# Kernel optimization log

Hardware: AMD Instinct MI355X
Metric: run time of the kernel (lower is better)

## Reference

```python
import jax, jax.numpy as jnp
import numpy as np

B, IN, H = 4096, 1024, 1024

def setup_inputs() -> dict:
    key = jax.random.key(0)
    ks = jax.random.split(key, 7)
    s_in = 1.0 / np.sqrt(IN)
    s_h = 1.0 / np.sqrt(H)
    return {
        "x": jax.random.normal(ks[0], (B, IN), dtype=jnp.float32),
        "h": jax.random.normal(ks[1], (B, H), dtype=jnp.float32),
        "W_ih": jax.random.uniform(ks[2], (3 * H, IN), jnp.float32, -s_in, s_in),
        "b_ih": jax.random.uniform(ks[3], (3 * H,), jnp.float32, -s_in, s_in),
        "W_rzh": jax.random.uniform(ks[4], (2 * H, H), jnp.float32, -s_h, s_h),
        "W_nh": jax.random.uniform(ks[5], (H, H), jnp.float32, -s_h, s_h),
        "b_nh": jax.random.uniform(ks[6], (H,), jnp.float32, -s_h, s_h),
    }


def reference(x, h, W_ih, b_ih, W_rzh, W_nh, b_nh):
    # Input projection: one fused matmul producing (B, 3H)
    x_proj = x @ W_ih.T + b_ih
    r_x, z_x, n_x = jnp.split(x_proj, 3, axis=-1)
    # Fused r/z hidden projection (B, 2H)
    rz_h = h @ W_rzh.T
    r_h, z_h = jnp.split(rz_h, 2, axis=-1)
    r = jax.nn.sigmoid(r_x + r_h)
    z = jax.nn.sigmoid(z_x + z_h)
    n = jnp.tanh(n_x + r * (h @ W_nh.T + b_nh))
    return (1.0 - z) * n + z * h
```

## Files before the change

### kernel.cpp

```cpp
#include <hip/hip_runtime.h>
#include <hip/hip_bf16.h>
#include <stdint.h>


typedef __attribute__((ext_vector_type(4))) int i32x4;
typedef __attribute__((ext_vector_type(16))) int i32x16;

#define SX (127.0f / 5.5f)
#define SW 4064.0f
#define INVS (1.0f / (SX * SW))

__device__ __forceinline__ unsigned pack4(const float4 f, float s) {
  int a = __float2int_rn(fminf(fmaxf(f.x * s, -127.f), 127.f));
  int b = __float2int_rn(fminf(fmaxf(f.y * s, -127.f), 127.f));
  int c = __float2int_rn(fminf(fmaxf(f.z * s, -127.f), 127.f));
  int d = __float2int_rn(fminf(fmaxf(f.w * s, -127.f), 127.f));
  return (unsigned)(a & 255) | ((unsigned)(b & 255) << 8) |
         ((unsigned)(c & 255) << 16) | ((unsigned)(d & 255) << 24);
}

__device__ __forceinline__ void cvt16(const float* __restrict__ src, float s,
                                      uint8_t* __restrict__ dst) {
  uint4 o;
  o.x = pack4(((const float4*)src)[0], s);
  o.y = pack4(((const float4*)src)[1], s);
  o.z = pack4(((const float4*)src)[2], s);
  o.w = pack4(((const float4*)src)[3], s);
  *(uint4*)dst = o;
}

__device__ __forceinline__ void load_lds16(const void* g, void* l) {
  __builtin_amdgcn_global_load_lds(
      (const __attribute__((address_space(1))) void*)g,
      (__attribute__((address_space(3))) void*)l, 16, 0, 0);
}

__global__ void prep_all(const float* __restrict__ x, const float* __restrict__ h,
                         const float* __restrict__ W_ih, const float* __restrict__ W_rzh,
                         const float* __restrict__ W_nh,
                         uint8_t* __restrict__ A2t, uint8_t* __restrict__ Wbt) {
  int ci = blockIdx.x * blockDim.x + threadIdx.x;
  if (ci < 524288) {
    int L = ci & 63;
    int kc = (ci >> 6) & 31;
    int win = (ci >> 11) & 1;
    int T = ci >> 12;
    int row = T * 32 + (L & 31);
    int col = kc * 32 + (L >> 5) * 16;
    const float* src = (win ? h : x) + (size_t)row * 1024 + col;
    cvt16(src, SX, A2t + (size_t)ci * 16);
  } else {
    int d = ci - 524288;
    int L = d & 63;
    int kc = (d >> 6) & 31;
    int rest = d >> 11;
    int bn = rest / 6;
    int item = rest - bn * 6;
    int jc = bn * 32 + (L & 31);
    int col = kc * 32 + (L >> 5) * 16;
    const float* src;
    switch (item) {
      case 0:  src = W_ih  + (size_t)jc * 1024 + col; break;
      case 1:  src = W_ih  + (size_t)(1024 + jc) * 1024 + col; break;
      case 2:  src = W_ih  + (size_t)(2048 + jc) * 1024 + col; break;
      case 3:  src = W_rzh + (size_t)jc * 1024 + col; break;
      case 4:  src = W_rzh + (size_t)(1024 + jc) * 1024 + col; break;
      default: src = W_nh  + (size_t)jc * 1024 + col; break;
    }
    cvt16(src, SW, Wbt + (size_t)d * 16);
  }
}

#define BODY(J, CUR, NXT)                                                        \
  {                                                                              \
    const int it = it2 * 2 + (J);                                                \
    __syncthreads();   \
    if (it < 15) {                                                               \
      const size_t go = (size_t)(it + 1) * 2048;                                 \
      _Pragma("unroll")                                                          \
      for (int i = 0; i < 3; ++i)                                                \
        load_lds16(gB[i] + go, &ldsB[((J) ^ 1) * 12288 + ldstB[i]]);             \
      NXT[0] = *(const i32x4*)(gax + go);                                        \
      NXT[1] = *(const i32x4*)(gax + go + 1024);                                 \
      NXT[2] = *(const i32x4*)(gah + go);                                        \
      NXT[3] = *(const i32x4*)(gah + go + 1024);                                 \
    }                                                                            \
    _Pragma("unroll")                                                            \
    for (int kcl = 0; kcl < 2; ++kcl) {                                          \
      const i32x4 ax = CUR[kcl];                                                 \
      const i32x4 ah = CUR[2 + kcl];                                             \
      i32x4 b0 = *(const i32x4*)&ldsB[(J) * 12288 + (0 * 2 + kcl) * 1024 + fo];  \
      i32x4 b1 = *(const i32x4*)&ldsB[(J) * 12288 + (1 * 2 + kcl) * 1024 + fo];  \
      i32x4 b2 = *(const i32x4*)&ldsB[(J) * 12288 + (2 * 2 + kcl) * 1024 + fo];  \
      acc[0] = __builtin_amdgcn_mfma_i32_32x32x32_i8(ax, b0, acc[0], 0, 0, 0);   \
      acc[1] = __builtin_amdgcn_mfma_i32_32x32x32_i8(ax, b1, acc[1], 0, 0, 0);   \
      acc[2] = __builtin_amdgcn_mfma_i32_32x32x32_i8(ax, b2, acc[2], 0, 0, 0);   \
      b0 = *(const i32x4*)&ldsB[(J) * 12288 + (3 * 2 + kcl) * 1024 + fo];        \
      b1 = *(const i32x4*)&ldsB[(J) * 12288 + (4 * 2 + kcl) * 1024 + fo];        \
      b2 = *(const i32x4*)&ldsB[(J) * 12288 + (5 * 2 + kcl) * 1024 + fo];        \
      acc[0] = __builtin_amdgcn_mfma_i32_32x32x32_i8(ah, b0, acc[0], 0, 0, 0);   \
      acc[1] = __builtin_amdgcn_mfma_i32_32x32x32_i8(ah, b1, acc[1], 0, 0, 0);   \
      acc[3] = __builtin_amdgcn_mfma_i32_32x32x32_i8(ah, b2, acc[3], 0, 0, 0);   \
    }                                                                            \
  }

__global__ __launch_bounds__(256, 4)
void gru_gemm_pipe(const uint8_t* __restrict__ A2t,
                   const uint8_t* __restrict__ Wbt,
                   const float* __restrict__ h,
                   const float* __restrict__ b_ih,
                   const float* __restrict__ b_nh,
                   float* __restrict__ out) {
  __shared__ uint8_t ldsB[2 * 12 * 1024];

  const int lane = threadIdx.x & 63;
  const int wave = threadIdx.x >> 6;
  const int m32 = lane & 31;
  const int khalf = lane >> 5;

  const int id = blockIdx.x;
  const int xcd = id & 7;
  const int rr = id >> 3;
  const int mg = (xcd >> 1) * 8 + (rr & 7);
  const int bn = (xcd & 1) * 16 + (rr >> 3);

  const int T = mg * 4 + wave;

  const uint8_t* gax = A2t + (size_t)(T * 2 + 0) * 32768 + lane * 16;
  const uint8_t* gah = A2t + (size_t)(T * 2 + 1) * 32768 + lane * 16;

  const uint8_t* gB[3];
  int ldstB[3];
#pragma unroll
  for (int i = 0; i < 3; ++i) {
    int c = wave * 3 + i;
    int item = c >> 1;
    int kcl = c & 1;
    gB[i] = Wbt + (size_t)(bn * 6 + item) * 32768 + kcl * 1024 + lane * 16;
    ldstB[i] = c * 1024 + lane * 16;
  }

  i32x16 acc[4] = {};
  const int fo = lane * 16;

  i32x4 aregA[4], aregB[4];

#pragma unroll
  for (int i = 0; i < 3; ++i) load_lds16(gB[i], &ldsB[ldstB[i]]);
  aregA[0] = *(const i32x4*)(gax);
  aregA[1] = *(const i32x4*)(gax + 1024);
  aregA[2] = *(const i32x4*)(gah);
  aregA[3] = *(const i32x4*)(gah + 1024);

#pragma unroll
  for (int it2 = 0; it2 < 8; ++it2) {
    BODY(0, aregA, aregB);
    BODY(1, aregB, aregA);
  }

  const int jcol = bn * 32 + m32;
  const float br  = b_ih[jcol];
  const float bz  = b_ih[1024 + jcol];
  const float bnv = b_ih[2048 + jcol];
  const float bh  = b_nh[jcol];
  const int row0 = mg * 128 + wave * 32;

#pragma unroll
  for (int i = 0; i < 16; ++i) {
    int mrow = row0 + (i & 3) + ((i >> 2) << 3) + (khalf << 2);
    size_t off = (size_t)mrow * 1024 + jcol;
    float pr = (float)acc[0][i] * INVS + br;
    float pz = (float)acc[1][i] * INVS + bz;
    float pn = (float)acc[2][i] * INVS + bnv;
    float ph = (float)acc[3][i] * INVS + bh;
    float rg = 1.f / (1.f + __expf(-pr));
    float zg = 1.f / (1.f + __expf(-pz));
    float e2 = __expf(2.f * (pn + rg * ph));
    float ng = 1.f - 2.f / (e2 + 1.f);
    float hv = h[off];
    out[off] = ng + zg * (hv - ng);
  }
}

extern "C" void kernel_launch(void* const* d_in, const int* in_sizes, int n_in,
                              void* d_out, int out_size, void* d_ws, size_t ws_size,
                              hipStream_t stream) {
  const float* x     = (const float*)d_in[0];
  const float* h     = (const float*)d_in[1];
  const float* W_ih  = (const float*)d_in[2];
  const float* b_ih  = (const float*)d_in[3];
  const float* W_rzh = (const float*)d_in[4];
  const float* W_nh  = (const float*)d_in[5];
  const float* b_nh  = (const float*)d_in[6];
  float* out = (float*)d_out;

  uint8_t* A2t = (uint8_t*)d_ws;
  uint8_t* Wbt = A2t + (size_t)524288 * 16;

  prep_all<<<dim3(3584), dim3(256), 0, stream>>>(x, h, W_ih, W_rzh, W_nh, A2t, Wbt);
  gru_gemm_pipe<<<dim3(1024), dim3(256), 0, stream>>>(A2t, Wbt, h, b_ih, b_nh, out);
}
```

Baseline: 140.4 us.

## Replace LDS double-buffered weight staging with direct global loads per wave

Removes the shared-memory double buffer and its global_load_lds prefetch and __syncthreads barriers. Each wave now loads its int8 activation and weight fragments straight from global memory (L2/L1) in a fully unrolled 32-step K loop. The intent is to drop barrier and LDS overhead and rely on the cache for weight reuse across the block's waves. The cost is redundant global traffic, since all four waves fetch the same weights, and possible exposed latency without explicit prefetching.

```diff
diff --git a/kernel.cpp b/kernel.cpp
--- a/kernel.cpp
+++ b/kernel.cpp
@@ -27,12 +27,6 @@
   o.z = pack4(((const float4*)src)[2], s);
   o.w = pack4(((const float4*)src)[3], s);
   *(uint4*)dst = o;
-}
-
-__device__ __forceinline__ void load_lds16(const void* g, void* l) {
-  __builtin_amdgcn_global_load_lds(
-      (const __attribute__((address_space(1))) void*)g,
-      (__attribute__((address_space(3))) void*)l, 16, 0, 0);
 }
 
 __global__ void prep_all(const float* __restrict__ x, const float* __restrict__ h,
@@ -71,39 +65,6 @@
   }
 }
 
-#define BODY(J, CUR, NXT)                                                        \
-  {                                                                              \
-    const int it = it2 * 2 + (J);                                                \
-    __syncthreads();   \
-    if (it < 15) {                                                               \
-      const size_t go = (size_t)(it + 1) * 2048;                                 \
-      _Pragma("unroll")                                                          \
-      for (int i = 0; i < 3; ++i)                                                \
-        load_lds16(gB[i] + go, &ldsB[((J) ^ 1) * 12288 + ldstB[i]]);             \
-      NXT[0] = *(const i32x4*)(gax + go);                                        \
-      NXT[1] = *(const i32x4*)(gax + go + 1024);                                 \
-      NXT[2] = *(const i32x4*)(gah + go);                                        \
-      NXT[3] = *(const i32x4*)(gah + go + 1024);                                 \
-    }                                                                            \
-    _Pragma("unroll")                                                            \
-    for (int kcl = 0; kcl < 2; ++kcl) {                                          \
-      const i32x4 ax = CUR[kcl];                                                 \
-      const i32x4 ah = CUR[2 + kcl];                                             \
-      i32x4 b0 = *(const i32x4*)&ldsB[(J) * 12288 + (0 * 2 + kcl) * 1024 + fo];  \
-      i32x4 b1 = *(const i32x4*)&ldsB[(J) * 12288 + (1 * 2 + kcl) * 1024 + fo];  \
-      i32x4 b2 = *(const i32x4*)&ldsB[(J) * 12288 + (2 * 2 + kcl) * 1024 + fo];  \
-      acc[0] = __builtin_amdgcn_mfma_i32_32x32x32_i8(ax, b0, acc[0], 0, 0, 0);   \
-      acc[1] = __builtin_amdgcn_mfma_i32_32x32x32_i8(ax, b1, acc[1], 0, 0, 0);   \
-      acc[2] = __builtin_amdgcn_mfma_i32_32x32x32_i8(ax, b2, acc[2], 0, 0, 0);   \
-      b0 = *(const i32x4*)&ldsB[(J) * 12288 + (3 * 2 + kcl) * 1024 + fo];        \
-      b1 = *(const i32x4*)&ldsB[(J) * 12288 + (4 * 2 + kcl) * 1024 + fo];        \
-      b2 = *(const i32x4*)&ldsB[(J) * 12288 + (5 * 2 + kcl) * 1024 + fo];        \
-      acc[0] = __builtin_amdgcn_mfma_i32_32x32x32_i8(ah, b0, acc[0], 0, 0, 0);   \
-      acc[1] = __builtin_amdgcn_mfma_i32_32x32x32_i8(ah, b1, acc[1], 0, 0, 0);   \
-      acc[3] = __builtin_amdgcn_mfma_i32_32x32x32_i8(ah, b2, acc[3], 0, 0, 0);   \
-    }                                                                            \
-  }
-
 __global__ __launch_bounds__(256, 4)
 void gru_gemm_pipe(const uint8_t* __restrict__ A2t,
                    const uint8_t* __restrict__ Wbt,
@@ -111,8 +72,6 @@
                    const float* __restrict__ b_ih,
                    const float* __restrict__ b_nh,
                    float* __restrict__ out) {
-  __shared__ uint8_t ldsB[2 * 12 * 1024];
-
   const int lane = threadIdx.x & 63;
   const int wave = threadIdx.x >> 6;
   const int m32 = lane & 31;
@@ -126,36 +85,28 @@
 
   const int T = mg * 4 + wave;
 
-  const uint8_t* gax = A2t + (size_t)(T * 2 + 0) * 32768 + lane * 16;
-  const uint8_t* gah = A2t + (size_t)(T * 2 + 1) * 32768 + lane * 16;
-
-  const uint8_t* gB[3];
-  int ldstB[3];
-#pragma unroll
-  for (int i = 0; i < 3; ++i) {
-    int c = wave * 3 + i;
-    int item = c >> 1;
-    int kcl = c & 1;
-    gB[i] = Wbt + (size_t)(bn * 6 + item) * 32768 + kcl * 1024 + lane * 16;
-    ldstB[i] = c * 1024 + lane * 16;
-  }
+  const uint8_t* gA = A2t + (size_t)(T * 2) * 32768 + (size_t)lane * 16;
+  const uint8_t* gW = Wbt + (size_t)(bn * 6) * 32768 + (size_t)lane * 16;
 
   i32x16 acc[4] = {};
-  const int fo = lane * 16;
-
-  i32x4 aregA[4], aregB[4];
 
 #pragma unroll
-  for (int i = 0; i < 3; ++i) load_lds16(gB[i], &ldsB[ldstB[i]]);
-  aregA[0] = *(const i32x4*)(gax);
-  aregA[1] = *(const i32x4*)(gax + 1024);
-  aregA[2] = *(const i32x4*)(gah);
-  aregA[3] = *(const i32x4*)(gah + 1024);
-
-#pragma unroll
-  for (int it2 = 0; it2 < 8; ++it2) {
-    BODY(0, aregA, aregB);
-    BODY(1, aregB, aregA);
+  for (int kc = 0; kc < 32; ++kc) {
+    const size_t o = (size_t)kc * 1024;
+    const i32x4 ax = *(const i32x4*)(gA + o);
+    const i32x4 ah = *(const i32x4*)(gA + 32768 + o);
+    const i32x4 b0 = *(const i32x4*)(gW + 0 * 32768 + o);
+    const i32x4 b1 = *(const i32x4*)(gW + 1 * 32768 + o);
+    const i32x4 b2 = *(const i32x4*)(gW + 2 * 32768 + o);
+    const i32x4 b3 = *(const i32x4*)(gW + 3 * 32768 + o);
+    const i32x4 b4 = *(const i32x4*)(gW + 4 * 32768 + o);
+    const i32x4 b5 = *(const i32x4*)(gW + 5 * 32768 + o);
+    acc[0] = __builtin_amdgcn_mfma_i32_32x32x32_i8(ax, b0, acc[0], 0, 0, 0);
+    acc[1] = __builtin_amdgcn_mfma_i32_32x32x32_i8(ax, b1, acc[1], 0, 0, 0);
+    acc[2] = __builtin_amdgcn_mfma_i32_32x32x32_i8(ax, b2, acc[2], 0, 0, 0);
+    acc[0] = __builtin_amdgcn_mfma_i32_32x32x32_i8(ah, b3, acc[0], 0, 0, 0);
+    acc[1] = __builtin_amdgcn_mfma_i32_32x32x32_i8(ah, b4, acc[1], 0, 0, 0);
+    acc[3] = __builtin_amdgcn_mfma_i32_32x32x32_i8(ah, b5, acc[3], 0, 0, 0);
   }
 
   const int jcol = bn * 32 + m32;
```

Measured after the change: 144.4 us. +2.8%, slower.
